# Kernel tuning notes

Measured on AMD Instinct MI355X. Metric: run time of the kernel, lower is better.

The kernel has to match this reference:

```python
import jax, jax.numpy as jnp
import numpy as np

B, C, NA = 32, 9, 65440
GAMMA = 3.0
SCALE_XY = 1.0 / 0.1
SCALE_WH = 1.0 / 0.2


def setup_inputs() -> dict:
    key = jax.random.key(0)
    k1, k2, k3, k4, k5 = jax.random.split(key, 5)
    bbox_delta = jax.random.normal(k1, (B, 4, NA), dtype=jnp.float32)
    confs = jax.random.normal(k2, (B, C, NA), dtype=jnp.float32)
    # gt boxes in xywh, keep w/h strictly positive for the log() in _loc_vec
    gt_bbox = jax.random.uniform(k3, (B, NA, 4), dtype=jnp.float32, minval=0.05, maxval=1.0)
    gt_labels = jax.random.randint(k4, (B, NA), 0, C, dtype=jnp.int32)
    anchors = jax.random.uniform(k5, (1, 4, NA), dtype=jnp.float32, minval=0.1, maxval=1.0)
    return {"bbox_delta": bbox_delta, "confs": confs, "gt_bbox": gt_bbox,
            "gt_labels": gt_labels, "anchors": anchors}


def reference(bbox_delta, confs, gt_bbox, gt_labels, anchors):
    n_classes = confs.shape[1]
    # ---- focal classification loss (fused: no one-hot materialized) ----
    # alpha = [10, 1000, ..., 1000]; einsum 'a,bcd->bad' followed by sum(dim=1)
    # collapses to multiplying by sum(alpha) since y is one-hot over c.
    alpha = jnp.full((n_classes,), 1000.0, dtype=jnp.float32).at[0].set(10.0)
    logp = jax.nn.log_softmax(confs, axis=1)              # [B,C,N]
    t = gt_labels.astype(jnp.int32)[:, None, :]           # [B,1,N]
    logp_t = jnp.take_along_axis(logp, t, axis=1)[:, 0, :]  # [B,N]
    p_t = jnp.exp(logp_t)
    focal = (1.0 - p_t) ** GAMMA * logp_t                 # [B,N]
    classification_loss = jnp.mean(-jnp.sum(alpha) * focal)

    # ---- localization loss (masked smooth-L1, no boolean compaction) ----
    gt_t = jnp.transpose(gt_bbox, (0, 2, 1))               # [B,4,N]
    gxy = SCALE_XY * (gt_t[:, :2, :] - anchors[:, :2, :]) / anchors[:, 2:, :]
    gwh = SCALE_WH * jnp.log(gt_t[:, 2:, :] / anchors[:, 2:, :])
    gt_loc = jnp.concatenate([gxy, gwh], axis=1)           # [B,4,N]

    pos = gt_labels > 0                                    # [B,N]
    mask = pos[:, None, :]                                 # broadcast over 4 coords
    diff = jnp.where(mask, bbox_delta - gt_loc, 0.0)
    ad = jnp.abs(diff)
    sl1 = jnp.where(ad < 1.0, 0.5 * diff * diff, ad - 0.5)
    regression_loss = jnp.sum(jnp.where(mask, sl1, 0.0))
    num_pos = jnp.sum(pos).astype(jnp.float32)

    total_loss = regression_loss / num_pos + classification_loss
    return total_loss
```

## Files before the change

### kernel.cpp

```cpp
#include <hip/hip_runtime.h>
#include <math.h>

constexpr int B  = 32;
constexpr int C  = 9;
constexpr int NA = 65440;
constexpr int PER_B    = NA / 4;
constexpr int NTHREADS = B * PER_B;
constexpr int BLOCK    = 256;
constexpr int GRID     = NTHREADS / BLOCK;

constexpr int WS_REG = 2048;
constexpr int WS_POS = 4096;

typedef float f4 __attribute__((ext_vector_type(4)));
typedef int   i4 __attribute__((ext_vector_type(4)));

__device__ __forceinline__ f4 ldnt(const float* p) {
    return __builtin_nontemporal_load(reinterpret_cast<const f4*>(p));
}
__device__ __forceinline__ i4 ldnti(const int* p) {
    return __builtin_nontemporal_load(reinterpret_cast<const i4*>(p));
}

__device__ __forceinline__ float smooth_l1(float d) {
    float ad = fabsf(d);
    return ad < 1.0f ? 0.5f * d * d : ad - 0.5f;
}

__global__ __launch_bounds__(BLOCK, 4) void ssd_main(
    const float* __restrict__ bbox_delta,
    const float* __restrict__ confs,
    const float* __restrict__ gt_bbox,
    const int*   __restrict__ gt_labels,
    const float* __restrict__ anchors,
    float* __restrict__ ws)
{
    const int tid = blockIdx.x * BLOCK + threadIdx.x;
    const int b   = tid / PER_B;
    const int a   = (tid - b * PER_B) * 4;

    const float* cbase = confs + (size_t)b * C * NA + a;
    f4 cf0 = ldnt(cbase);
    f4 cf1 = ldnt(cbase + 1 * NA);
    f4 cf2 = ldnt(cbase + 2 * NA);
    f4 cf3 = ldnt(cbase + 3 * NA);
    f4 cf4 = ldnt(cbase + 4 * NA);
    f4 cf5 = ldnt(cbase + 5 * NA);
    f4 cf6 = ldnt(cbase + 6 * NA);
    f4 cf7 = ldnt(cbase + 7 * NA);
    f4 cf8 = ldnt(cbase + 8 * NA);

    const i4 lab = ldnti(gt_labels + (size_t)b * NA + a);

    const float* abase = anchors + a;
    f4 ax = ldnt(abase);
    f4 ay = ldnt(abase + NA);
    f4 aw = ldnt(abase + 2 * NA);
    f4 ah = ldnt(abase + 3 * NA);

    const float* dbase = bbox_delta + (size_t)b * 4 * NA + a;
    f4 d0 = ldnt(dbase);
    f4 d1 = ldnt(dbase + NA);
    f4 d2 = ldnt(dbase + 2 * NA);
    f4 d3 = ldnt(dbase + 3 * NA);

    const float* gbase = gt_bbox + ((size_t)b * NA + a) * 4;
    f4 g0 = ldnt(gbase);
    f4 g1 = ldnt(gbase + 4);
    f4 g2 = ldnt(gbase + 8);
    f4 g3 = ldnt(gbase + 12);

    __builtin_amdgcn_sched_barrier(0);

    f4 cf[C] = {cf0, cf1, cf2, cf3, cf4, cf5, cf6, cf7, cf8};
    float sex = 0.f, sey = 0.f, sez = 0.f, sew = 0.f;
    float ctx = cf0[0], cty = cf0[1], ctz = cf0[2], ctw = cf0[3];
#pragma unroll
    for (int c = 0; c < C; ++c) {
        sex += __expf(cf[c][0]);
        sey += __expf(cf[c][1]);
        sez += __expf(cf[c][2]);
        sew += __expf(cf[c][3]);
        ctx = (lab[0] == c) ? cf[c][0] : ctx;
        cty = (lab[1] == c) ? cf[c][1] : cty;
        ctz = (lab[2] == c) ? cf[c][2] : ctz;
        ctw = (lab[3] == c) ? cf[c][3] : ctw;
    }
    float lpx = ctx - __logf(sex);
    float lpy = cty - __logf(sey);
    float lpz = ctz - __logf(sez);
    float lpw = ctw - __logf(sew);

    float focal;
    {
        float px = __expf(lpx), py = __expf(lpy), pz = __expf(lpz), pw = __expf(lpw);
        float ox = 1.f - px, oy = 1.f - py, oz = 1.f - pz, ow = 1.f - pw;
        focal = ox*ox*ox*lpx + oy*oy*oy*lpy + oz*oz*oz*lpz + ow*ow*ow*lpw;
    }

    float reg = 0.f, pcnt = 0.f;
#define DO_ANCHOR(K)                                                              \
    {                                                                             \
        float gx = 10.0f * __fdividef(g##K[0] - ax[K], aw[K]);                    \
        float gy = 10.0f * __fdividef(g##K[1] - ay[K], ah[K]);                    \
        float gw = 5.0f * __logf(__fdividef(g##K[2], aw[K]));                     \
        float gh = 5.0f * __logf(__fdividef(g##K[3], ah[K]));                     \
        float s  = smooth_l1(d0[K] - gx) + smooth_l1(d1[K] - gy) +                \
                   smooth_l1(d2[K] - gw) + smooth_l1(d3[K] - gh);                 \
        if (lab[K] > 0) { reg += s; pcnt += 1.0f; }                               \
    }
    DO_ANCHOR(0)
    DO_ANCHOR(1)
    DO_ANCHOR(2)
    DO_ANCHOR(3)
#undef DO_ANCHOR

#pragma unroll
    for (int off = 32; off > 0; off >>= 1) {
        focal += __shfl_down(focal, off, 64);
        reg   += __shfl_down(reg,   off, 64);
        pcnt  += __shfl_down(pcnt,  off, 64);
    }
    __shared__ float sf[4], sr[4], sp[4];
    const int wid  = threadIdx.x >> 6;
    const int lane = threadIdx.x & 63;
    if (lane == 0) { sf[wid] = focal; sr[wid] = reg; sp[wid] = pcnt; }
    __syncthreads();
    if (threadIdx.x == 0) {
        ws[blockIdx.x]          = sf[0] + sf[1] + sf[2] + sf[3];
        ws[WS_REG + blockIdx.x] = sr[0] + sr[1] + sr[2] + sr[3];
        ws[WS_POS + blockIdx.x] = sp[0] + sp[1] + sp[2] + sp[3];
    }
}

__global__ __launch_bounds__(256) void finalize_k(const float* __restrict__ ws,
                                                  float* __restrict__ out) {
    float F = 0.f, R = 0.f, P = 0.f;
    for (int i = threadIdx.x; i < GRID; i += 256) {
        F += ws[i];
        R += ws[WS_REG + i];
        P += ws[WS_POS + i];
    }
#pragma unroll
    for (int off = 32; off > 0; off >>= 1) {
        F += __shfl_down(F, off, 64);
        R += __shfl_down(R, off, 64);
        P += __shfl_down(P, off, 64);
    }
    __shared__ float sf[4], sr[4], sp[4];
    const int wid  = threadIdx.x >> 6;
    const int lane = threadIdx.x & 63;
    if (lane == 0) { sf[wid] = F; sr[wid] = R; sp[wid] = P; }
    __syncthreads();
    if (threadIdx.x == 0) {
        float Ft = sf[0] + sf[1] + sf[2] + sf[3];
        float Rt = sr[0] + sr[1] + sr[2] + sr[3];
        float Pt = sp[0] + sp[1] + sp[2] + sp[3];
        const float inv_n = 1.0f / (float)((size_t)B * NA);
        out[0] = Rt / Pt - 8010.0f * Ft * inv_n;
    }
}

extern "C" void kernel_launch(void* const* d_in, const int* in_sizes, int n_in,
                              void* d_out, int out_size, void* d_ws, size_t ws_size,
                              hipStream_t stream) {
    const float* bbox_delta = (const float*)d_in[0];
    const float* confs      = (const float*)d_in[1];
    const float* gt_bbox    = (const float*)d_in[2];
    const int*   gt_labels  = (const int*)d_in[3];
    const float* anchors    = (const float*)d_in[4];
    float* ws  = (float*)d_ws;
    float* out = (float*)d_out;

    ssd_main<<<GRID, BLOCK, 0, stream>>>(bbox_delta, confs, gt_bbox, gt_labels, anchors, ws);
    finalize_k<<<1, 256, 0, stream>>>(ws, out);
}
```

Baseline: 165.3 us.

## Use persistent grid-stride loop with software-prefetched confs and LDS-transposed gt_bbox loads

```diff
diff --git a/kernel.cpp b/kernel.cpp
--- a/kernel.cpp
+++ b/kernel.cpp
@@ -4,10 +4,11 @@
 constexpr int B  = 32;
 constexpr int C  = 9;
 constexpr int NA = 65440;
-constexpr int PER_B    = NA / 4;
-constexpr int NTHREADS = B * PER_B;
-constexpr int BLOCK    = 256;
-constexpr int GRID     = NTHREADS / BLOCK;
+constexpr int PER_B  = NA / 4;
+constexpr int NTOT   = B * PER_B;
+constexpr int BLOCK  = 256;
+constexpr int GRID   = 512;
+constexpr int STRIDE = GRID * BLOCK;
 
 constexpr int WS_REG = 2048;
 constexpr int WS_POS = 4096;
@@ -21,13 +22,16 @@
 __device__ __forceinline__ i4 ldnti(const int* p) {
     return __builtin_nontemporal_load(reinterpret_cast<const i4*>(p));
 }
-
+__device__ __forceinline__ f4 ld4(const float* p) {
+    return *reinterpret_cast<const f4*>(p);
+}
 __device__ __forceinline__ float smooth_l1(float d) {
     float ad = fabsf(d);
     return ad < 1.0f ? 0.5f * d * d : ad - 0.5f;
 }
-
-__global__ __launch_bounds__(BLOCK, 4) void ssd_main(
+__device__ __forceinline__ int swz(int i) { return i ^ ((i >> 3) & 7); }
+
+__global__ __launch_bounds__(BLOCK, 2) void ssd_main(
     const float* __restrict__ bbox_delta,
     const float* __restrict__ confs,
     const float* __restrict__ gt_bbox,
@@ -35,96 +39,125 @@
     const float* __restrict__ anchors,
     float* __restrict__ ws)
 {
-    const int tid = blockIdx.x * BLOCK + threadIdx.x;
-    const int b   = tid / PER_B;
-    const int a   = (tid - b * PER_B) * 4;
-
-    const float* cbase = confs + (size_t)b * C * NA + a;
-    f4 cf0 = ldnt(cbase);
-    f4 cf1 = ldnt(cbase + 1 * NA);
-    f4 cf2 = ldnt(cbase + 2 * NA);
-    f4 cf3 = ldnt(cbase + 3 * NA);
-    f4 cf4 = ldnt(cbase + 4 * NA);
-    f4 cf5 = ldnt(cbase + 5 * NA);
-    f4 cf6 = ldnt(cbase + 6 * NA);
-    f4 cf7 = ldnt(cbase + 7 * NA);
-    f4 cf8 = ldnt(cbase + 8 * NA);
-
-    const i4 lab = ldnti(gt_labels + (size_t)b * NA + a);
-
-    const float* abase = anchors + a;
-    f4 ax = ldnt(abase);
-    f4 ay = ldnt(abase + NA);
-    f4 aw = ldnt(abase + 2 * NA);
-    f4 ah = ldnt(abase + 3 * NA);
-
-    const float* dbase = bbox_delta + (size_t)b * 4 * NA + a;
-    f4 d0 = ldnt(dbase);
-    f4 d1 = ldnt(dbase + NA);
-    f4 d2 = ldnt(dbase + 2 * NA);
-    f4 d3 = ldnt(dbase + 3 * NA);
-
-    const float* gbase = gt_bbox + ((size_t)b * NA + a) * 4;
-    f4 g0 = ldnt(gbase);
-    f4 g1 = ldnt(gbase + 4);
-    f4 g2 = ldnt(gbase + 8);
-    f4 g3 = ldnt(gbase + 12);
-
+    __shared__ f4 gswz[4][256];
+
+    const int lane = threadIdx.x & 63;
+    const int wid  = threadIdx.x >> 6;
+    const f4* gt4  = reinterpret_cast<const f4*>(gt_bbox);
+
+    float facc = 0.f, racc = 0.f, pacc = 0.f;
+
+    int i = blockIdx.x * BLOCK + threadIdx.x;
+    int b = i / PER_B;
+    int a = (i - b * PER_B) * 4;
+    f4 cf0, cf1, cf2, cf3, cf4, cf5, cf6, cf7, cf8; i4 lab;
+    {
+        const float* cb = confs + (size_t)b * C * NA + a;
+        cf0 = ldnt(cb);          cf1 = ldnt(cb + 1 * NA); cf2 = ldnt(cb + 2 * NA);
+        cf3 = ldnt(cb + 3 * NA); cf4 = ldnt(cb + 4 * NA); cf5 = ldnt(cb + 5 * NA);
+        cf6 = ldnt(cb + 6 * NA); cf7 = ldnt(cb + 7 * NA); cf8 = ldnt(cb + 8 * NA);
+        lab = ldnti(gt_labels + (size_t)b * NA + a);
+    }
     __builtin_amdgcn_sched_barrier(0);
 
-    f4 cf[C] = {cf0, cf1, cf2, cf3, cf4, cf5, cf6, cf7, cf8};
-    float sex = 0.f, sey = 0.f, sez = 0.f, sew = 0.f;
-    float ctx = cf0[0], cty = cf0[1], ctz = cf0[2], ctw = cf0[3];
+    f4 ncf0 = {0,0,0,0}, ncf1 = ncf0, ncf2 = ncf0, ncf3 = ncf0, ncf4 = ncf0,
+       ncf5 = ncf0, ncf6 = ncf0, ncf7 = ncf0, ncf8 = ncf0;
+    i4 nlab = {0,0,0,0};
+
+    while (true) {
+        const int iw = i - lane;
+        const size_t gb = (size_t)4 * iw;
+        f4 gv0 = ldnt(reinterpret_cast<const float*>(gt4 + gb + 0 * 64 + lane));
+        f4 gv1 = ldnt(reinterpret_cast<const float*>(gt4 + gb + 1 * 64 + lane));
+        f4 gv2 = ldnt(reinterpret_cast<const float*>(gt4 + gb + 2 * 64 + lane));
+        f4 gv3 = ldnt(reinterpret_cast<const float*>(gt4 + gb + 3 * 64 + lane));
+        const float* db = bbox_delta + (size_t)b * 4 * NA + a;
+        f4 d0 = ldnt(db);          f4 d1 = ldnt(db + NA);
+        f4 d2 = ldnt(db + 2 * NA); f4 d3 = ldnt(db + 3 * NA);
+        const float* ab = anchors + a;
+        f4 ax = ld4(ab);          f4 ay = ld4(ab + NA);
+        f4 aw = ld4(ab + 2 * NA); f4 ah = ld4(ab + 3 * NA);
+        __builtin_amdgcn_sched_barrier(0);
+
+        {
+            f4 cf[C] = {cf0, cf1, cf2, cf3, cf4, cf5, cf6, cf7, cf8};
+            float sex = 0.f, sey = 0.f, sez = 0.f, sew = 0.f;
+            float ctx = cf0[0], cty = cf0[1], ctz = cf0[2], ctw = cf0[3];
 #pragma unroll
-    for (int c = 0; c < C; ++c) {
-        sex += __expf(cf[c][0]);
-        sey += __expf(cf[c][1]);
-        sez += __expf(cf[c][2]);
-        sew += __expf(cf[c][3]);
-        ctx = (lab[0] == c) ? cf[c][0] : ctx;
-        cty = (lab[1] == c) ? cf[c][1] : cty;
-        ctz = (lab[2] == c) ? cf[c][2] : ctz;
-        ctw = (lab[3] == c) ? cf[c][3] : ctw;
-    }
-    float lpx = ctx - __logf(sex);
-    float lpy = cty - __logf(sey);
-    float lpz = ctz - __logf(sez);
-    float lpw = ctw - __logf(sew);
-
-    float focal;
-    {
-        float px = __expf(lpx), py = __expf(lpy), pz = __expf(lpz), pw = __expf(lpw);
-        float ox = 1.f - px, oy = 1.f - py, oz = 1.f - pz, ow = 1.f - pw;
-        focal = ox*ox*ox*lpx + oy*oy*oy*lpy + oz*oz*oz*lpz + ow*ow*ow*lpw;
-    }
-
-    float reg = 0.f, pcnt = 0.f;
+            for (int c = 0; c < C; ++c) {
+                sex += __expf(cf[c][0]);
+                sey += __expf(cf[c][1]);
+                sez += __expf(cf[c][2]);
+                sew += __expf(cf[c][3]);
+                ctx = (lab[0] == c) ? cf[c][0] : ctx;
+                cty = (lab[1] == c) ? cf[c][1] : cty;
+                ctz = (lab[2] == c) ? cf[c][2] : ctz;
+                ctw = (lab[3] == c) ? cf[c][3] : ctw;
+            }
+            float lpx = ctx - __logf(sex);
+            float lpy = cty - __logf(sey);
+            float lpz = ctz - __logf(sez);
+            float lpw = ctw - __logf(sew);
+            float px = __expf(lpx), py = __expf(lpy), pz = __expf(lpz), pw = __expf(lpw);
+            float ox = 1.f - px, oy = 1.f - py, oz = 1.f - pz, ow = 1.f - pw;
+            facc += ox*ox*ox*lpx + oy*oy*oy*lpy + oz*oz*oz*lpz + ow*ow*ow*lpw;
+        }
+        __builtin_amdgcn_sched_barrier(0);
+
+        const int inext = i + STRIDE;
+        const bool more = (inext < NTOT);
+        int bn = 0, an = 0;
+        if (more) {
+            bn = inext / PER_B;
+            an = (inext - bn * PER_B) * 4;
+            const float* cbn = confs + (size_t)bn * C * NA + an;
+            ncf0 = ldnt(cbn);          ncf1 = ldnt(cbn + 1 * NA); ncf2 = ldnt(cbn + 2 * NA);
+            ncf3 = ldnt(cbn + 3 * NA); ncf4 = ldnt(cbn + 4 * NA); ncf5 = ldnt(cbn + 5 * NA);
+            ncf6 = ldnt(cbn + 6 * NA); ncf7 = ldnt(cbn + 7 * NA); ncf8 = ldnt(cbn + 8 * NA);
+            nlab = ldnti(gt_labels + (size_t)bn * NA + an);
+        }
+        __builtin_amdgcn_sched_barrier(0);
+
+        gswz[wid][swz(0 * 64 + lane)] = gv0;
+        gswz[wid][swz(1 * 64 + lane)] = gv1;
+        gswz[wid][swz(2 * 64 + lane)] = gv2;
+        gswz[wid][swz(3 * 64 + lane)] = gv3;
+        const int i0 = lane << 2;
+        f4 g0 = gswz[wid][swz(i0 + 0)];
+        f4 g1 = gswz[wid][swz(i0 + 1)];
+        f4 g2 = gswz[wid][swz(i0 + 2)];
+        f4 g3 = gswz[wid][swz(i0 + 3)];
+
 #define DO_ANCHOR(K)                                                              \
-    {                                                                             \
-        float gx = 10.0f * __fdividef(g##K[0] - ax[K], aw[K]);                    \
-        float gy = 10.0f * __fdividef(g##K[1] - ay[K], ah[K]);                    \
-        float gw = 5.0f * __logf(__fdividef(g##K[2], aw[K]));                     \
-        float gh = 5.0f * __logf(__fdividef(g##K[3], ah[K]));                     \
-        float s  = smooth_l1(d0[K] - gx) + smooth_l1(d1[K] - gy) +                \
-                   smooth_l1(d2[K] - gw) + smooth_l1(d3[K] - gh);                 \
-        if (lab[K] > 0) { reg += s; pcnt += 1.0f; }                               \
-    }
-    DO_ANCHOR(0)
-    DO_ANCHOR(1)
-    DO_ANCHOR(2)
-    DO_ANCHOR(3)
+        {                                                                         \
+            float gx = 10.0f * __fdividef(g##K[0] - ax[K], aw[K]);                \
+            float gy = 10.0f * __fdividef(g##K[1] - ay[K], ah[K]);                \
+            float gw = 5.0f * __logf(__fdividef(g##K[2], aw[K]));                 \
+            float gh = 5.0f * __logf(__fdividef(g##K[3], ah[K]));                 \
+            float s  = smooth_l1(d0[K] - gx) + smooth_l1(d1[K] - gy) +            \
+                       smooth_l1(d2[K] - gw) + smooth_l1(d3[K] - gh);             \
+            if (lab[K] > 0) { racc += s; pacc += 1.0f; }                          \
+        }
+        DO_ANCHOR(0)
+        DO_ANCHOR(1)
+        DO_ANCHOR(2)
+        DO_ANCHOR(3)
 #undef DO_ANCHOR
+
+        if (!more) break;
+        i = inext; b = bn; a = an;
+        cf0 = ncf0; cf1 = ncf1; cf2 = ncf2; cf3 = ncf3; cf4 = ncf4;
+        cf5 = ncf5; cf6 = ncf6; cf7 = ncf7; cf8 = ncf8; lab = nlab;
+    }
 
 #pragma unroll
     for (int off = 32; off > 0; off >>= 1) {
-        focal += __shfl_down(focal, off, 64);
-        reg   += __shfl_down(reg,   off, 64);
-        pcnt  += __shfl_down(pcnt,  off, 64);
+        facc += __shfl_down(facc, off, 64);
+        racc += __shfl_down(racc, off, 64);
+        pacc += __shfl_down(pacc, off, 64);
     }
     __shared__ float sf[4], sr[4], sp[4];
-    const int wid  = threadIdx.x >> 6;
-    const int lane = threadIdx.x & 63;
-    if (lane == 0) { sf[wid] = focal; sr[wid] = reg; sp[wid] = pcnt; }
+    if (lane == 0) { sf[wid] = facc; sr[wid] = racc; sp[wid] = pacc; }
     __syncthreads();
     if (threadIdx.x == 0) {
         ws[blockIdx.x]          = sf[0] + sf[1] + sf[2] + sf[3];
```

After: 162.0 us. -2.0%, faster.
